# Performance work log

Hardware: AMD Instinct MI355X
Metric: run time of the kernel (lower is better)

## Reference

```python
import jax, jax.numpy as jnp
import numpy as np

N = 100000      # nodes
E = 1600000     # edges (avg degree 16)
H = 128         # hidden channels
L = 5           # num_layers (only valid range 4<num_layers<8 for this module; 4 index-errors)
ALPHA = 0.1
THETA = 0.5
EPS = 1e-5      # BatchNorm1d default eps


def setup_inputs() -> dict:
    key = jax.random.key(0)
    ks = jax.random.split(key, 8)
    x = jax.random.normal(ks[0], (N, H), dtype=jnp.float32)
    W_in = jax.random.normal(ks[1], (H, H), dtype=jnp.float32) / np.float32(np.sqrt(H))
    b_in = jnp.zeros((H,), jnp.float32)
    conv_W = jax.random.normal(ks[2], (L, H, H), dtype=jnp.float32) / np.float32(np.sqrt(H))
    bn_gamma = jnp.ones((L - 1, H), jnp.float32)
    bn_beta = jnp.zeros((L - 1, H), jnp.float32)
    W_jk = jax.random.normal(ks[3], (4 * H, H), dtype=jnp.float32) / np.float32(np.sqrt(4 * H))
    b_jk = jnp.zeros((H,), jnp.float32)
    src = jax.random.randint(ks[4], (E,), 0, N, dtype=jnp.int32).astype(jnp.int64)
    dst = jax.random.randint(ks[5], (E,), 0, N, dtype=jnp.int32).astype(jnp.int64)
    return dict(x=x, W_in=W_in, b_in=b_in, conv_W=conv_W, bn_gamma=bn_gamma,
                bn_beta=bn_beta, W_jk=W_jk, b_jk=b_jk, src=src, dst=dst)


def _batchnorm(z, gamma, beta):
    # BatchNorm1d, training-mode batch statistics over the node dimension
    m = z.mean(axis=0)
    v = z.var(axis=0)
    return (z - m) * jax.lax.rsqrt(v + EPS) * gamma + beta


def reference(x, W_in, b_in, conv_W, bn_gamma, bn_beta, W_jk, b_jk, src, dst):
    # lins[0]
    z = x @ W_in + b_in          # [N, H]
    x0 = z                       # initial residual for GCNII
    zs = []
    for i in range(L):
        # GCN2Conv (shared_weights=True, normalize=False):
        #   msg = A @ z  (sparse propagation over edge list)
        msg = jax.ops.segment_sum(z[src], dst, num_segments=N)   # [N, H]
        h = (1.0 - ALPHA) * msg + ALPHA * x0
        beta_l = float(np.log(THETA / (i + 1) + 1.0))
        z = (1.0 - beta_l) * h + beta_l * (h @ conv_W[i])
        zs.append(z)
        if i % 4 == 3:
            # JumpingKnowledge('cat') over the 4 layer outputs, then lins[-1].
            # (Original code also applies BN here but immediately overwrites z,
            #  so that BN is dead computation and is skipped.)
            z = jnp.concatenate(zs[:4], axis=-1) @ W_jk + b_jk   # [N, H]
        elif i < L - 1:
            z = jax.nn.relu(_batchnorm(z, bn_gamma[i], bn_beta[i]))
    return z
```

## Files before the change

### kernel.cpp

```cpp
#include <hip/hip_runtime.h>
#include <hip/hip_bf16.h>
#include <cmath>
#include <cstddef>

#define NN 100000
#define HH 128
#define EE 1600000
#define NH (NN * HH)
#define ALPHA_C 0.1f
#define THETA_C 0.5f
#define EPS_C 1e-5f

constexpr int TR = 64;
constexpr int AST = 68;
constexpr int SCAN_B = 256;
constexpr int NBLK = (NN + SCAN_B - 1) / SCAN_B;

__global__ __launch_bounds__(256) void zero_int_k(int* __restrict__ p, int n) {
    int i = blockIdx.x * 256 + threadIdx.x;
    if (i < n) p[i] = 0;
}
__global__ __launch_bounds__(256) void zero_f4_k(float4* __restrict__ p, int n4) {
    int i = blockIdx.x * 256 + threadIdx.x;
    if (i < n4) p[i] = float4{0.f, 0.f, 0.f, 0.f};
}

__global__ void detect_idx64(const int* __restrict__ p, int* __restrict__ flag) {
    int any = 0;
    for (int i = 0; i < 64; ++i) any |= p[2 * i + 1];
    *flag = (any == 0) ? 1 : 0;
}

__device__ __forceinline__ int load_idx(const void* p, int e, int is64) {
    return is64 ? (int)((const long long*)p)[e] : ((const int*)p)[e];
}

__global__ __launch_bounds__(256) void hist_k(
    const void* __restrict__ dstp, const int* __restrict__ flag,
    int* __restrict__ hist)
{
    int e = blockIdx.x * 256 + threadIdx.x;
    if (e >= EE) return;
    atomicAdd(&hist[load_idx(dstp, e, *flag)], 1);
}

__global__ __launch_bounds__(SCAN_B) void scan1_k(
    const int* __restrict__ hist, int* __restrict__ incl, int* __restrict__ bsum)
{
    __shared__ int sh[SCAN_B];
    int t = threadIdx.x;
    int i = blockIdx.x * SCAN_B + t;
    int v = (i < NN) ? hist[i] : 0;
    sh[t] = v;
    __syncthreads();
    for (int off = 1; off < SCAN_B; off <<= 1) {
        int x = (t >= off) ? sh[t - off] : 0;
        __syncthreads();
        sh[t] += x;
        __syncthreads();
    }
    if (i < NN) incl[i] = sh[t];
    if (t == SCAN_B - 1) bsum[blockIdx.x] = sh[t];
}

__global__ __launch_bounds__(512) void scan2_k(int* __restrict__ bsum) {
    __shared__ int sh[512];
    int t = threadIdx.x;
    sh[t] = (t < NBLK) ? bsum[t] : 0;
    __syncthreads();
    for (int off = 1; off < 512; off <<= 1) {
        int x = (t >= off) ? sh[t - off] : 0;
        __syncthreads();
        sh[t] += x;
        __syncthreads();
    }
    if (t < NBLK) bsum[t] = sh[t];
}

__global__ __launch_bounds__(SCAN_B) void scan3_k(
    const int* __restrict__ hist, const int* __restrict__ incl,
    const int* __restrict__ bsum, int* __restrict__ row_ptr,
    int* __restrict__ cursor)
{
    int b = blockIdx.x;
    int i = b * SCAN_B + threadIdx.x;
    if (i < NN) {
        int ex = incl[i] - hist[i] + (b > 0 ? bsum[b - 1] : 0);
        row_ptr[i] = ex;
        cursor[i] = ex;
    }
    if (i == 0) row_ptr[NN] = EE;
}

__global__ __launch_bounds__(256) void fill_k(
    const void* __restrict__ srcp, const void* __restrict__ dstp,
    const int* __restrict__ flag, int* __restrict__ cursor,
    int* __restrict__ sorted_src)
{
    int e = blockIdx.x * 256 + threadIdx.x;
    if (e >= EE) return;
    int is64 = *flag;
    int d = load_idx(dstp, e, is64);
    int pos = atomicAdd(&cursor[d], 1);
    sorted_src[pos] = load_idx(srcp, e, is64);
}

__global__ __launch_bounds__(256) void prep_w(
    const float* __restrict__ W_in, const float* __restrict__ conv_W,
    float* __restrict__ Wp)
{
    int i = blockIdx.y;
    int idx = blockIdx.x * 256 + threadIdx.x;
    float v;
    if (i == 0) {
        v = W_in[idx];
    } else {
        float bl = logf(THETA_C / (float)i + 1.f);
        int k = idx >> 7, c = idx & 127;
        v = bl * conv_W[(size_t)(i - 1) * 16384 + idx] + ((k == c) ? (1.f - bl) : 0.f);
    }
    Wp[(size_t)i * 16384 + idx] = v;
}

__global__ __launch_bounds__(256, 4) void gemm128(
    const float* __restrict__ A, const float* __restrict__ Wp,
    const float* __restrict__ bias, float* __restrict__ out,
    float* __restrict__ statsp, int nrows)
{
    __shared__ float As[HH * AST];
    const int t = threadIdx.x;
    const int tx = t & 31;
    const int ty = t >> 5;
    const int lane = t & 63, w = t >> 6;
    const int row0 = blockIdx.x * TR;

#pragma unroll
    for (int i = 0; i < 8; ++i) {
        int r = (i & 3) * 16 + (lane & 15);
        int k4 = ((i >> 2) * 4 + w) * 4 + (lane >> 4);
        float4 v = {0.f, 0.f, 0.f, 0.f};
        if (row0 + r < nrows)
            v = ((const float4*)(A + (size_t)(row0 + r) * HH))[k4];
        int k = k4 * 4;
        As[(k + 0) * AST + r] = v.x;
        As[(k + 1) * AST + r] = v.y;
        As[(k + 2) * AST + r] = v.z;
        As[(k + 3) * AST + r] = v.w;
    }
    __syncthreads();

    float acc[8][4];
#pragma unroll
    for (int ii = 0; ii < 8; ++ii)
#pragma unroll
        for (int j = 0; j < 4; ++j) acc[ii][j] = 0.f;

    const float4* W4 = (const float4*)Wp;
    float4 wbuf[4];
#pragma unroll
    for (int kk = 0; kk < 4; ++kk) wbuf[kk] = W4[kk * 32 + tx];

    for (int k0 = 0; k0 < HH; k0 += 4) {
        float4 wn[4];
        const bool more = (k0 + 4 < HH);
#pragma unroll
        for (int kk = 0; kk < 4; ++kk) {
            if (more) wn[kk] = W4[(k0 + 4 + kk) * 32 + tx];
            int k = k0 + kk;
            const float* ap = &As[k * AST + ty * 8];
            float4 a0 = *(const float4*)ap;
            float4 a1 = *(const float4*)(ap + 4);
            float a[8] = {a0.x, a0.y, a0.z, a0.w, a1.x, a1.y, a1.z, a1.w};
#pragma unroll
            for (int ii = 0; ii < 8; ++ii) {
                acc[ii][0] += a[ii] * wbuf[kk].x;
                acc[ii][1] += a[ii] * wbuf[kk].y;
                acc[ii][2] += a[ii] * wbuf[kk].z;
                acc[ii][3] += a[ii] * wbuf[kk].w;
            }
        }
        if (more) {
#pragma unroll
            for (int kk = 0; kk < 4; ++kk) wbuf[kk] = wn[kk];
        }
    }

    float4 b4 = {0.f, 0.f, 0.f, 0.f};
    if (bias) b4 = ((const float4*)bias)[tx];
#pragma unroll
    for (int ii = 0; ii < 8; ++ii) {
        int r = row0 + ty * 8 + ii;
        if (r < nrows) {
            float4 v = {acc[ii][0] + b4.x, acc[ii][1] + b4.y,
                        acc[ii][2] + b4.z, acc[ii][3] + b4.w};
            ((float4*)out)[(size_t)r * 32 + tx] = v;
        }
    }
    (void)statsp;
}

template <bool BN, bool DOSTATS>
__global__ __launch_bounds__(256, 2) void fused_layer(
    const float* __restrict__ z, const int* __restrict__ row_ptr,
    const int* __restrict__ sorted_src,
    const float* __restrict__ stats,
    const float* __restrict__ gamma, const float* __restrict__ beta,
    const float* __restrict__ resid,
    const float* __restrict__ Wp, float* __restrict__ out,
    float* __restrict__ statsp, int nrows)
{
    __shared__ float As[HH * AST];
    const int t = threadIdx.x;
    const int tx = t & 31;
    const int ty = t >> 5;
    const int lane = t & 63, w = t >> 6;
    const int row0 = blockIdx.x * TR;

    const int half = lane >> 5;
    const int c4 = lane & 31;

    float4 sc = {1.f, 1.f, 1.f, 1.f}, sh = {0.f, 0.f, 0.f, 0.f};
    if (BN) {
        const float invN = 1.f / (float)NN;
        float4 s  = ((const float4*)stats)[c4];
        float4 s2 = ((const float4*)(stats + 128))[c4];
        float4 g  = ((const float4*)gamma)[c4];
        float4 b  = ((const float4*)beta)[c4];
        float m, var;
        m = s.x * invN; var = s2.x * invN - m * m;
        sc.x = rsqrtf(var + EPS_C) * g.x; sh.x = b.x - m * sc.x;
        m = s.y * invN; var = s2.y * invN - m * m;
        sc.y = rsqrtf(var + EPS_C) * g.y; sh.y = b.y - m * sc.y;
        m = s.z * invN; var = s2.z * invN - m * m;
        sc.z = rsqrtf(var + EPS_C) * g.z; sh.z = b.z - m * sc.z;
        m = s.w * invN; var = s2.w * invN - m * m;
        sc.w = rsqrtf(var + EPS_C) * g.w; sh.w = b.w - m * sc.w;
    }

    for (int i = 0; i < 16; ++i) {
        int rr = w * 16 + i;
        int node = row0 + rr;
        if (node < nrows) {
            float4 r4v = ((const float4*)(resid + (size_t)node * HH))[c4];
            int e1 = row_ptr[node + 1];
            int e = row_ptr[node] + half;
            float4 acc  = {0.f, 0.f, 0.f, 0.f};
            float4 acc2 = {0.f, 0.f, 0.f, 0.f};
            float4 acc3 = {0.f, 0.f, 0.f, 0.f};
            float4 acc4 = {0.f, 0.f, 0.f, 0.f};
            for (; e + 6 < e1; e += 8) {
                int s0 = sorted_src[e];
                int s1 = sorted_src[e + 2];
                int s2 = sorted_src[e + 4];
                int s3 = sorted_src[e + 6];
                float4 v0 = ((const float4*)(z + (size_t)s0 * HH))[c4];
                float4 v1 = ((const float4*)(z + (size_t)s1 * HH))[c4];
                float4 v2 = ((const float4*)(z + (size_t)s2 * HH))[c4];
                float4 v3 = ((const float4*)(z + (size_t)s3 * HH))[c4];
                if (BN) {
                    v0.x = fmaxf(0.f, v0.x * sc.x + sh.x);
                    v0.y = fmaxf(0.f, v0.y * sc.y + sh.y);
                    v0.z = fmaxf(0.f, v0.z * sc.z + sh.z);
                    v0.w = fmaxf(0.f, v0.w * sc.w + sh.w);
                    v1.x = fmaxf(0.f, v1.x * sc.x + sh.x);
                    v1.y = fmaxf(0.f, v1.y * sc.y + sh.y);
                    v1.z = fmaxf(0.f, v1.z * sc.z + sh.z);
                    v1.w = fmaxf(0.f, v1.w * sc.w + sh.w);
                    v2.x = fmaxf(0.f, v2.x * sc.x + sh.x);
                    v2.y = fmaxf(0.f, v2.y * sc.y + sh.y);
                    v2.z = fmaxf(0.f, v2.z * sc.z + sh.z);
                    v2.w = fmaxf(0.f, v2.w * sc.w + sh.w);
                    v3.x = fmaxf(0.f, v3.x * sc.x + sh.x);
                    v3.y = fmaxf(0.f, v3.y * sc.y + sh.y);
                    v3.z = fmaxf(0.f, v3.z * sc.z + sh.z);
                    v3.w = fmaxf(0.f, v3.w * sc.w + sh.w);
                }
                acc.x  += v0.x; acc.y  += v0.y; acc.z  += v0.z; acc.w  += v0.w;
                acc2.x += v1.x; acc2.y += v1.y; acc2.z += v1.z; acc2.w += v1.w;
                acc3.x += v2.x; acc3.y += v2.y; acc3.z += v2.z; acc3.w += v2.w;
                acc4.x += v3.x; acc4.y += v3.y; acc4.z += v3.z; acc4.w += v3.w;
            }
            for (; e + 2 < e1; e += 4) {
                int s0 = sorted_src[e];
                int s1 = sorted_src[e + 2];
                float4 v0 = ((const float4*)(z + (size_t)s0 * HH))[c4];
                float4 v1 = ((const float4*)(z + (size_t)s1 * HH))[c4];
                if (BN) {
                    v0.x = fmaxf(0.f, v0.x * sc.x + sh.x);
                    v0.y = fmaxf(0.f, v0.y * sc.y + sh.y);
                    v0.z = fmaxf(0.f, v0.z * sc.z + sh.z);
                    v0.w = fmaxf(0.f, v0.w * sc.w + sh.w);
                    v1.x = fmaxf(0.f, v1.x * sc.x + sh.x);
                    v1.y = fmaxf(0.f, v1.y * sc.y + sh.y);
                    v1.z = fmaxf(0.f, v1.z * sc.z + sh.z);
                    v1.w = fmaxf(0.f, v1.w * sc.w + sh.w);
                }
                acc.x  += v0.x; acc.y  += v0.y; acc.z  += v0.z; acc.w  += v0.w;
                acc2.x += v1.x; acc2.y += v1.y; acc2.z += v1.z; acc2.w += v1.w;
            }
            if (e < e1) {
                int s = sorted_src[e];
                float4 v = ((const float4*)(z + (size_t)s * HH))[c4];
                if (BN) {
                    v.x = fmaxf(0.f, v.x * sc.x + sh.x);
                    v.y = fmaxf(0.f, v.y * sc.y + sh.y);
                    v.z = fmaxf(0.f, v.z * sc.z + sh.z);
                    v.w = fmaxf(0.f, v.w * sc.w + sh.w);
                }
                acc.x += v.x; acc.y += v.y; acc.z += v.z; acc.w += v.w;
            }
            acc.x += acc2.x + acc3.x + acc4.x;
            acc.y += acc2.y + acc3.y + acc4.y;
            acc.z += acc2.z + acc3.z + acc4.z;
            acc.w += acc2.w + acc3.w + acc4.w;
            acc.x += __shfl_down(acc.x, 32);
            acc.y += __shfl_down(acc.y, 32);
            acc.z += __shfl_down(acc.z, 32);
            acc.w += __shfl_down(acc.w, 32);
            if (half == 0) {
                const float cA = 1.f - ALPHA_C, cB = ALPHA_C;
                int k = c4 * 4;
                As[(k + 0) * AST + rr] = cA * acc.x + cB * r4v.x;
                As[(k + 1) * AST + rr] = cA * acc.y + cB * r4v.y;
                As[(k + 2) * AST + rr] = cA * acc.z + cB * r4v.z;
                As[(k + 3) * AST + rr] = cA * acc.w + cB * r4v.w;
            }
        }
    }
    __syncthreads();

    float acc[8][4];
#pragma unroll
    for (int ii = 0; ii < 8; ++ii)
#pragma unroll
        for (int j = 0; j < 4; ++j) acc[ii][j] = 0.f;

    const float4* W4 = (const float4*)Wp;
    float4 wbuf[4];
#pragma unroll
    for (int kk = 0; kk < 4; ++kk) wbuf[kk] = W4[kk * 32 + tx];

    for (int k0 = 0; k0 < HH; k0 += 4) {
        float4 wn[4];
        const bool more = (k0 + 4 < HH);
#pragma unroll
        for (int kk = 0; kk < 4; ++kk) {
            if (more) wn[kk] = W4[(k0 + 4 + kk) * 32 + tx];
            int k = k0 + kk;
            const float* ap = &As[k * AST + ty * 8];
            float4 a0 = *(const float4*)ap;
            float4 a1 = *(const float4*)(ap + 4);
            float a[8] = {a0.x, a0.y, a0.z, a0.w, a1.x, a1.y, a1.z, a1.w};
#pragma unroll
            for (int ii = 0; ii < 8; ++ii) {
                acc[ii][0] += a[ii] * wbuf[kk].x;
                acc[ii][1] += a[ii] * wbuf[kk].y;
                acc[ii][2] += a[ii] * wbuf[kk].z;
                acc[ii][3] += a[ii] * wbuf[kk].w;
            }
        }
        if (more) {
#pragma unroll
            for (int kk = 0; kk < 4; ++kk) wbuf[kk] = wn[kk];
        }
    }

    float cs[4] = {0.f, 0.f, 0.f, 0.f}, cq[4] = {0.f, 0.f, 0.f, 0.f};
#pragma unroll
    for (int ii = 0; ii < 8; ++ii) {
        int r = row0 + ty * 8 + ii;
        if (r < nrows) {
            float4 v = {acc[ii][0], acc[ii][1], acc[ii][2], acc[ii][3]};
            ((float4*)out)[(size_t)r * 32 + tx] = v;
            if (DOSTATS) {
                cs[0] += v.x; cq[0] += v.x * v.x;
                cs[1] += v.y; cq[1] += v.y * v.y;
                cs[2] += v.z; cq[2] += v.z * v.z;
                cs[3] += v.w; cq[3] += v.w * v.w;
            }
        }
    }
    if (DOSTATS) {
        __syncthreads();
        float* red = As;
#pragma unroll
        for (int j = 0; j < 4; ++j) {
            red[ty * 128 + tx * 4 + j] = cs[j];
            red[1024 + ty * 128 + tx * 4 + j] = cq[j];
        }
        __syncthreads();
        if (t < 128) {
            float s = 0.f, q = 0.f;
#pragma unroll
            for (int g = 0; g < 8; ++g) {
                s += red[g * 128 + t];
                q += red[1024 + g * 128 + t];
            }
            atomicAdd(&statsp[t], s);
            atomicAdd(&statsp[128 + t], q);
        }
    }
}

__global__ __launch_bounds__(256, 4) void gemm_jk(
    const float* __restrict__ z0, const float* __restrict__ z1,
    const float* __restrict__ z2, const float* __restrict__ z3,
    const float* __restrict__ Wjk, const float* __restrict__ bjk,
    float* __restrict__ out, int nrows)
{
    __shared__ float As[HH * AST];
    const int t = threadIdx.x;
    const int tx = t & 31;
    const int ty = t >> 5;
    const int lane = t & 63, w = t >> 6;
    const int row0 = blockIdx.x * TR;

    float acc[8][4];
#pragma unroll
    for (int ii = 0; ii < 8; ++ii)
#pragma unroll
        for (int j = 0; j < 4; ++j) acc[ii][j] = 0.f;

    const float* srcs[4] = {z0, z1, z2, z3};
    for (int j = 0; j < 4; ++j) {
        if (j) __syncthreads();
        const float* Z = srcs[j];
#pragma unroll
        for (int i = 0; i < 8; ++i) {
            int r = (i & 3) * 16 + (lane & 15);
            int k4 = ((i >> 2) * 4 + w) * 4 + (lane >> 4);
            float4 v = {0.f, 0.f, 0.f, 0.f};
            if (row0 + r < nrows)
                v = ((const float4*)(Z + (size_t)(row0 + r) * HH))[k4];
            int k = k4 * 4;
            As[(k + 0) * AST + r] = v.x;
            As[(k + 1) * AST + r] = v.y;
            As[(k + 2) * AST + r] = v.z;
            As[(k + 3) * AST + r] = v.w;
        }
        __syncthreads();

        const float4* W4 = (const float4*)(Wjk + (size_t)j * 128 * HH);
        float4 wbuf[4];
#pragma unroll
        for (int kk = 0; kk < 4; ++kk) wbuf[kk] = W4[kk * 32 + tx];

        for (int k0 = 0; k0 < HH; k0 += 4) {
            float4 wn[4];
            const bool more = (k0 + 4 < HH);
#pragma unroll
            for (int kk = 0; kk < 4; ++kk) {
                if (more) wn[kk] = W4[(k0 + 4 + kk) * 32 + tx];
                int k = k0 + kk;
                const float* ap = &As[k * AST + ty * 8];
                float4 a0 = *(const float4*)ap;
                float4 a1 = *(const float4*)(ap + 4);
                float a[8] = {a0.x, a0.y, a0.z, a0.w, a1.x, a1.y, a1.z, a1.w};
#pragma unroll
                for (int ii = 0; ii < 8; ++ii) {
                    acc[ii][0] += a[ii] * wbuf[kk].x;
                    acc[ii][1] += a[ii] * wbuf[kk].y;
                    acc[ii][2] += a[ii] * wbuf[kk].z;
                    acc[ii][3] += a[ii] * wbuf[kk].w;
                }
            }
            if (more) {
#pragma unroll
                for (int kk = 0; kk < 4; ++kk) wbuf[kk] = wn[kk];
            }
        }
    }

    float4 b4 = ((const float4*)bjk)[tx];
#pragma unroll
    for (int ii = 0; ii < 8; ++ii) {
        int r = row0 + ty * 8 + ii;
        if (r < nrows) {
            float4 v = {acc[ii][0] + b4.x, acc[ii][1] + b4.y,
                        acc[ii][2] + b4.z, acc[ii][3] + b4.w};
            ((float4*)out)[(size_t)r * 32 + tx] = v;
        }
    }
}

extern "C" void kernel_launch(void* const* d_in, const int* in_sizes, int n_in,
                              void* d_out, int out_size, void* d_ws, size_t ws_size,
                              hipStream_t stream)
{
    const float* x       = (const float*)d_in[0];
    const float* W_in    = (const float*)d_in[1];
    const float* b_in    = (const float*)d_in[2];
    const float* conv_W  = (const float*)d_in[3];
    const float* bn_g    = (const float*)d_in[4];
    const float* bn_b    = (const float*)d_in[5];
    const float* W_jk    = (const float*)d_in[6];
    const float* b_jk    = (const float*)d_in[7];
    const void*  srcp    = d_in[8];
    const void*  dstp    = d_in[9];

    float* ws     = (float*)d_ws;
    float* x0     = ws;
    float* msg    = ws + (size_t)NH;
    float* zs0    = ws + 2 * (size_t)NH;
    float* zs1    = ws + 3 * (size_t)NH;
    float* zs2    = ws + 4 * (size_t)NH;
    float* stats3 = ws + 5 * (size_t)NH;
    int*   flag       = (int*)(stats3 + 768);
    int*   hist       = flag + 1;
    int*   incl       = hist + NN;
    int*   row_ptr    = incl + NN;
    int*   cursor     = row_ptr + NN + 1;
    int*   bsum       = cursor + NN;
    int*   sorted_src = bsum + NBLK + 1;
    float* Wp         = (float*)(sorted_src + EE);
    (void)msg;

    const int GEMM_GRID = (NN + TR - 1) / TR;
    const int EDGE_GRID = (EE + 255) / 256;

    detect_idx64<<<1, 1, 0, stream>>>((const int*)srcp, flag);
    zero_int_k<<<(NN + 255) / 256, 256, 0, stream>>>(hist, NN);
    zero_f4_k<<<1, 192, 0, stream>>>((float4*)stats3, 192);
    hist_k<<<EDGE_GRID, 256, 0, stream>>>(dstp, flag, hist);
    scan1_k<<<NBLK, SCAN_B, 0, stream>>>(hist, incl, bsum);
    scan2_k<<<1, 512, 0, stream>>>(bsum);
    scan3_k<<<NBLK, SCAN_B, 0, stream>>>(hist, incl, bsum, row_ptr, cursor);
    fill_k<<<EDGE_GRID, 256, 0, stream>>>(srcp, dstp, flag, cursor, sorted_src);
    prep_w<<<dim3(64, 6), 256, 0, stream>>>(W_in, conv_W, Wp);

    gemm128<<<GEMM_GRID, 256, 0, stream>>>(x, Wp, b_in, x0, nullptr, NN);

    fused_layer<false, true><<<GEMM_GRID, 256, 0, stream>>>(
        x0, row_ptr, sorted_src, nullptr, nullptr, nullptr, x0,
        Wp + 1 * 16384, zs0, stats3 + 0, NN);
    fused_layer<true, true><<<GEMM_GRID, 256, 0, stream>>>(
        zs0, row_ptr, sorted_src, stats3 + 0, bn_g + 0, bn_b + 0, x0,
        Wp + 2 * 16384, zs1, stats3 + 256, NN);
    fused_layer<true, true><<<GEMM_GRID, 256, 0, stream>>>(
        zs1, row_ptr, sorted_src, stats3 + 256, bn_g + HH, bn_b + HH, x0,
        Wp + 3 * 16384, zs2, stats3 + 512, NN);
    fused_layer<true, false><<<GEMM_GRID, 256, 0, stream>>>(
        zs2, row_ptr, sorted_src, stats3 + 512, bn_g + 2 * HH, bn_b + 2 * HH, x0,
        Wp + 4 * 16384, (float*)d_out, nullptr, NN);
    gemm_jk<<<GEMM_GRID, 256, 0, stream>>>(zs0, zs1, zs2, (const float*)d_out,
                                           W_jk, b_jk, zs0, NN);
    fused_layer<false, false><<<GEMM_GRID, 256, 0, stream>>>(
        zs0, row_ptr, sorted_src, nullptr, nullptr, nullptr, x0,
        Wp + 5 * 16384, (float*)d_out, nullptr, NN);
}
```

Before: 1.435 ms.

## Fuse layer-3 propagation and GEMM with the JumpingKnowledge GEMM

Merges the fourth GCN2 layer (gather, BN+ReLU, residual mix, conv GEMM) and the JK concat GEMM into one kernel. The layer-3 result stays in shared memory and is multiplied by the last W_jk slice directly, so it is never written to and re-read from global memory, and one launch goes away. In exchange the fused kernel holds two accumulator tiles, which raises register pressure, and it is capped at two blocks per CU instead of four for the JK part. The output is written in place over zs0, which is safe only because each block reads its own zs0 rows before writing them.

```diff
diff --git a/kernel.cpp b/kernel.cpp
--- a/kernel.cpp
+++ b/kernel.cpp
@@ -198,6 +198,7 @@
     }
     (void)statsp;
 }
+
 
 template <bool BN, bool DOSTATS>
 __global__ __launch_bounds__(256, 2) void fused_layer(
@@ -402,11 +403,15 @@
     }
 }
 
-__global__ __launch_bounds__(256, 4) void gemm_jk(
+__global__ __launch_bounds__(256, 2) void fused_l3_jk(
+    const float* __restrict__ z, const int* __restrict__ row_ptr,
+    const int* __restrict__ sorted_src,
+    const float* __restrict__ stats, const float* __restrict__ gamma,
+    const float* __restrict__ beta, const float* __restrict__ resid,
+    const float* __restrict__ Wl,
     const float* __restrict__ z0, const float* __restrict__ z1,
-    const float* __restrict__ z2, const float* __restrict__ z3,
-    const float* __restrict__ Wjk, const float* __restrict__ bjk,
-    float* __restrict__ out, int nrows)
+    const float* __restrict__ z2, const float* __restrict__ Wjk,
+    const float* __restrict__ bjk, float* out, int nrows)
 {
     __shared__ float As[HH * AST];
     const int t = threadIdx.x;
@@ -414,16 +419,198 @@
     const int ty = t >> 5;
     const int lane = t & 63, w = t >> 6;
     const int row0 = blockIdx.x * TR;
+    const int half = lane >> 5;
+    const int c4 = lane & 31;
+
+    float4 sc, sh;
+    {
+        const float invN = 1.f / (float)NN;
+        float4 s  = ((const float4*)stats)[c4];
+        float4 s2 = ((const float4*)(stats + 128))[c4];
+        float4 g  = ((const float4*)gamma)[c4];
+        float4 b  = ((const float4*)beta)[c4];
+        float m, var;
+        m = s.x * invN; var = s2.x * invN - m * m;
+        sc.x = rsqrtf(var + EPS_C) * g.x; sh.x = b.x - m * sc.x;
+        m = s.y * invN; var = s2.y * invN - m * m;
+        sc.y = rsqrtf(var + EPS_C) * g.y; sh.y = b.y - m * sc.y;
+        m = s.z * invN; var = s2.z * invN - m * m;
+        sc.z = rsqrtf(var + EPS_C) * g.z; sh.z = b.z - m * sc.z;
+        m = s.w * invN; var = s2.w * invN - m * m;
+        sc.w = rsqrtf(var + EPS_C) * g.w; sh.w = b.w - m * sc.w;
+    }
+
+    for (int i = 0; i < 16; ++i) {
+        int rr = w * 16 + i;
+        int node = row0 + rr;
+        if (node < nrows) {
+            float4 r4v = ((const float4*)(resid + (size_t)node * HH))[c4];
+            int e1 = row_ptr[node + 1];
+            int e = row_ptr[node] + half;
+            float4 acc  = {0.f, 0.f, 0.f, 0.f};
+            float4 acc2 = {0.f, 0.f, 0.f, 0.f};
+            float4 acc3 = {0.f, 0.f, 0.f, 0.f};
+            float4 acc4 = {0.f, 0.f, 0.f, 0.f};
+            for (; e + 6 < e1; e += 8) {
+                int s0 = sorted_src[e];
+                int s1 = sorted_src[e + 2];
+                int s2 = sorted_src[e + 4];
+                int s3 = sorted_src[e + 6];
+                float4 v0 = ((const float4*)(z + (size_t)s0 * HH))[c4];
+                float4 v1 = ((const float4*)(z + (size_t)s1 * HH))[c4];
+                float4 v2 = ((const float4*)(z + (size_t)s2 * HH))[c4];
+                float4 v3 = ((const float4*)(z + (size_t)s3 * HH))[c4];
+                v0.x = fmaxf(0.f, v0.x * sc.x + sh.x);
+                v0.y = fmaxf(0.f, v0.y * sc.y + sh.y);
+                v0.z = fmaxf(0.f, v0.z * sc.z + sh.z);
+                v0.w = fmaxf(0.f, v0.w * sc.w + sh.w);
+                v1.x = fmaxf(0.f, v1.x * sc.x + sh.x);
+                v1.y = fmaxf(0.f, v1.y * sc.y + sh.y);
+                v1.z = fmaxf(0.f, v1.z * sc.z + sh.z);
+                v1.w = fmaxf(0.f, v1.w * sc.w + sh.w);
+                v2.x = fmaxf(0.f, v2.x * sc.x + sh.x);
+                v2.y = fmaxf(0.f, v2.y * sc.y + sh.y);
+                v2.z = fmaxf(0.f, v2.z * sc.z + sh.z);
+                v2.w = fmaxf(0.f, v2.w * sc.w + sh.w);
+                v3.x = fmaxf(0.f, v3.x * sc.x + sh.x);
+                v3.y = fmaxf(0.f, v3.y * sc.y + sh.y);
+                v3.z = fmaxf(0.f, v3.z * sc.z + sh.z);
+                v3.w = fmaxf(0.f, v3.w * sc.w + sh.w);
+                acc.x  += v0.x; acc.y  += v0.y; acc.z  += v0.z; acc.w  += v0.w;
+                acc2.x += v1.x; acc2.y += v1.y; acc2.z += v1.z; acc2.w += v1.w;
+                acc3.x += v2.x; acc3.y += v2.y; acc3.z += v2.z; acc3.w += v2.w;
+                acc4.x += v3.x; acc4.y += v3.y; acc4.z += v3.z; acc4.w += v3.w;
+            }
+            for (; e + 2 < e1; e += 4) {
+                int s0 = sorted_src[e];
+                int s1 = sorted_src[e + 2];
+                float4 v0 = ((const float4*)(z + (size_t)s0 * HH))[c4];
+                float4 v1 = ((const float4*)(z + (size_t)s1 * HH))[c4];
+                v0.x = fmaxf(0.f, v0.x * sc.x + sh.x);
+                v0.y = fmaxf(0.f, v0.y * sc.y + sh.y);
+                v0.z = fmaxf(0.f, v0.z * sc.z + sh.z);
+                v0.w = fmaxf(0.f, v0.w * sc.w + sh.w);
+                v1.x = fmaxf(0.f, v1.x * sc.x + sh.x);
+                v1.y = fmaxf(0.f, v1.y * sc.y + sh.y);
+                v1.z = fmaxf(0.f, v1.z * sc.z + sh.z);
+                v1.w = fmaxf(0.f, v1.w * sc.w + sh.w);
+                acc.x  += v0.x; acc.y  += v0.y; acc.z  += v0.z; acc.w  += v0.w;
+                acc2.x += v1.x; acc2.y += v1.y; acc2.z += v1.z; acc2.w += v1.w;
+            }
+            if (e < e1) {
+                int s = sorted_src[e];
+                float4 v = ((const float4*)(z + (size_t)s * HH))[c4];
+                v.x = fmaxf(0.f, v.x * sc.x + sh.x);
+                v.y = fmaxf(0.f, v.y * sc.y + sh.y);
+                v.z = fmaxf(0.f, v.z * sc.z + sh.z);
+                v.w = fmaxf(0.f, v.w * sc.w + sh.w);
+                acc.x += v.x; acc.y += v.y; acc.z += v.z; acc.w += v.w;
+            }
+            acc.x += acc2.x + acc3.x + acc4.x;
+            acc.y += acc2.y + acc3.y + acc4.y;
+            acc.z += acc2.z + acc3.z + acc4.z;
+            acc.w += acc2.w + acc3.w + acc4.w;
+            acc.x += __shfl_down(acc.x, 32);
+            acc.y += __shfl_down(acc.y, 32);
+            acc.z += __shfl_down(acc.z, 32);
+            acc.w += __shfl_down(acc.w, 32);
+            if (half == 0) {
+                const float cA = 1.f - ALPHA_C, cB = ALPHA_C;
+                int k = c4 * 4;
+                As[(k + 0) * AST + rr] = cA * acc.x + cB * r4v.x;
+                As[(k + 1) * AST + rr] = cA * acc.y + cB * r4v.y;
+                As[(k + 2) * AST + rr] = cA * acc.z + cB * r4v.z;
+                As[(k + 3) * AST + rr] = cA * acc.w + cB * r4v.w;
+            }
+        }
+    }
+    __syncthreads();
 
     float acc[8][4];
 #pragma unroll
     for (int ii = 0; ii < 8; ++ii)
 #pragma unroll
         for (int j = 0; j < 4; ++j) acc[ii][j] = 0.f;
-
-    const float* srcs[4] = {z0, z1, z2, z3};
-    for (int j = 0; j < 4; ++j) {
-        if (j) __syncthreads();
+    {
+        const float4* W4 = (const float4*)Wl;
+        float4 wbuf[4];
+#pragma unroll
+        for (int kk = 0; kk < 4; ++kk) wbuf[kk] = W4[kk * 32 + tx];
+        for (int k0 = 0; k0 < HH; k0 += 4) {
+            float4 wn[4];
+            const bool more = (k0 + 4 < HH);
+#pragma unroll
+            for (int kk = 0; kk < 4; ++kk) {
+                if (more) wn[kk] = W4[(k0 + 4 + kk) * 32 + tx];
+                int k = k0 + kk;
+                const float* ap = &As[k * AST + ty * 8];
+                float4 a0 = *(const float4*)ap;
+                float4 a1 = *(const float4*)(ap + 4);
+                float a[8] = {a0.x, a0.y, a0.z, a0.w, a1.x, a1.y, a1.z, a1.w};
+#pragma unroll
+                for (int ii = 0; ii < 8; ++ii) {
+                    acc[ii][0] += a[ii] * wbuf[kk].x;
+                    acc[ii][1] += a[ii] * wbuf[kk].y;
+                    acc[ii][2] += a[ii] * wbuf[kk].z;
+                    acc[ii][3] += a[ii] * wbuf[kk].w;
+                }
+            }
+            if (more) {
+#pragma unroll
+                for (int kk = 0; kk < 4; ++kk) wbuf[kk] = wn[kk];
+            }
+        }
+    }
+
+    __syncthreads();
+#pragma unroll
+    for (int ii = 0; ii < 8; ++ii) {
+#pragma unroll
+        for (int j = 0; j < 4; ++j)
+            As[(tx * 4 + j) * AST + ty * 8 + ii] = acc[ii][j];
+    }
+    __syncthreads();
+
+    float ajk[8][4];
+#pragma unroll
+    for (int ii = 0; ii < 8; ++ii)
+#pragma unroll
+        for (int j = 0; j < 4; ++j) ajk[ii][j] = 0.f;
+
+    {
+        const float4* W4 = (const float4*)(Wjk + (size_t)3 * 128 * HH);
+        float4 wbuf[4];
+#pragma unroll
+        for (int kk = 0; kk < 4; ++kk) wbuf[kk] = W4[kk * 32 + tx];
+        for (int k0 = 0; k0 < HH; k0 += 4) {
+            float4 wn[4];
+            const bool more = (k0 + 4 < HH);
+#pragma unroll
+            for (int kk = 0; kk < 4; ++kk) {
+                if (more) wn[kk] = W4[(k0 + 4 + kk) * 32 + tx];
+                int k = k0 + kk;
+                const float* ap = &As[k * AST + ty * 8];
+                float4 a0 = *(const float4*)ap;
+                float4 a1 = *(const float4*)(ap + 4);
+                float a[8] = {a0.x, a0.y, a0.z, a0.w, a1.x, a1.y, a1.z, a1.w};
+#pragma unroll
+                for (int ii = 0; ii < 8; ++ii) {
+                    ajk[ii][0] += a[ii] * wbuf[kk].x;
+                    ajk[ii][1] += a[ii] * wbuf[kk].y;
+                    ajk[ii][2] += a[ii] * wbuf[kk].z;
+                    ajk[ii][3] += a[ii] * wbuf[kk].w;
+                }
+            }
+            if (more) {
+#pragma unroll
+                for (int kk = 0; kk < 4; ++kk) wbuf[kk] = wn[kk];
+            }
+        }
+    }
+
+    const float* srcs[3] = {z0, z1, z2};
+    for (int j = 0; j < 3; ++j) {
+        __syncthreads();
         const float* Z = srcs[j];
 #pragma unroll
         for (int i = 0; i < 8; ++i) {
@@ -444,7 +631,6 @@
         float4 wbuf[4];
 #pragma unroll
         for (int kk = 0; kk < 4; ++kk) wbuf[kk] = W4[kk * 32 + tx];
-
         for (int k0 = 0; k0 < HH; k0 += 4) {
             float4 wn[4];
             const bool more = (k0 + 4 < HH);
@@ -458,10 +644,10 @@
                 float a[8] = {a0.x, a0.y, a0.z, a0.w, a1.x, a1.y, a1.z, a1.w};
 #pragma unroll
                 for (int ii = 0; ii < 8; ++ii) {
-                    acc[ii][0] += a[ii] * wbuf[kk].x;
-                    acc[ii][1] += a[ii] * wbuf[kk].y;
-                    acc[ii][2] += a[ii] * wbuf[kk].z;
-                    acc[ii][3] += a[ii] * wbuf[kk].w;
+                    ajk[ii][0] += a[ii] * wbuf[kk].x;
+                    ajk[ii][1] += a[ii] * wbuf[kk].y;
+                    ajk[ii][2] += a[ii] * wbuf[kk].z;
+                    ajk[ii][3] += a[ii] * wbuf[kk].w;
                 }
             }
             if (more) {
@@ -476,8 +662,8 @@
     for (int ii = 0; ii < 8; ++ii) {
         int r = row0 + ty * 8 + ii;
         if (r < nrows) {
-            float4 v = {acc[ii][0] + b4.x, acc[ii][1] + b4.y,
-                        acc[ii][2] + b4.z, acc[ii][3] + b4.w};
+            float4 v = {ajk[ii][0] + b4.x, ajk[ii][1] + b4.y,
+                        ajk[ii][2] + b4.z, ajk[ii][3] + b4.w};
             ((float4*)out)[(size_t)r * 32 + tx] = v;
         }
     }
@@ -500,7 +686,6 @@
 
     float* ws     = (float*)d_ws;
     float* x0     = ws;
-    float* msg    = ws + (size_t)NH;
     float* zs0    = ws + 2 * (size_t)NH;
     float* zs1    = ws + 3 * (size_t)NH;
     float* zs2    = ws + 4 * (size_t)NH;
@@ -513,7 +698,6 @@
     int*   bsum       = cursor + NN;
     int*   sorted_src = bsum + NBLK + 1;
     float* Wp         = (float*)(sorted_src + EE);
-    (void)msg;
 
     const int GEMM_GRID = (NN + TR - 1) / TR;
     const int EDGE_GRID = (EE + 255) / 256;
@@ -539,11 +723,9 @@
     fused_layer<true, true><<<GEMM_GRID, 256, 0, stream>>>(
         zs1, row_ptr, sorted_src, stats3 + 256, bn_g + HH, bn_b + HH, x0,
         Wp + 3 * 16384, zs2, stats3 + 512, NN);
-    fused_layer<true, false><<<GEMM_GRID, 256, 0, stream>>>(
-        zs2, row_ptr, sorted_src, stats3 + 512, bn_g + 2 * HH, bn_b + 2 * HH, x0,
-        Wp + 4 * 16384, (float*)d_out, nullptr, NN);
-    gemm_jk<<<GEMM_GRID, 256, 0, stream>>>(zs0, zs1, zs2, (const float*)d_out,
-                                           W_jk, b_jk, zs0, NN);
+    fused_l3_jk<<<GEMM_GRID, 256, 0, stream>>>(
+        zs2, row_ptr, sorted_src, stats3 + 512, bn_g + 2 * HH, bn_b + 2 * HH,
+        x0, Wp + 4 * 16384, zs0, zs1, zs2, W_jk, b_jk, zs0, NN);
     fused_layer<false, false><<<GEMM_GRID, 256, 0, stream>>>(
         zs0, row_ptr, sorted_src, nullptr, nullptr, nullptr, x0,
         Wp + 5 * 16384, (float*)d_out, nullptr, NN);
```

After: 1.488 ms. 1.04x slower.
